# Kernel optimization log

Hardware: AMD Instinct MI355X
Metric: run time of the kernel (lower is better)

## Reference

```python
import jax, jax.numpy as jnp
import numpy as np

N_USERS, N_MOVIES, D, E, C = 100000, 50000, 128, 1000000, 5


def setup_inputs() -> dict:
    key = jax.random.key(0)
    ks = jax.random.split(key, 6)
    ufeat = jax.random.normal(ks[0], (N_USERS, D), dtype=jnp.float32)
    ifeat = jax.random.normal(ks[1], (N_MOVIES, D), dtype=jnp.float32)
    # Xavier-uniform init, PyTorch Linear layout [out, in]
    b1 = float(np.sqrt(6.0 / (2 * D + D)))
    W1 = jax.random.uniform(ks[2], (D, 2 * D), dtype=jnp.float32, minval=-b1, maxval=b1)
    b2 = float(np.sqrt(6.0 / (D + C)))
    W2 = jax.random.uniform(ks[3], (C, D), dtype=jnp.float32, minval=-b2, maxval=b2)
    src_idx = jax.random.randint(ks[4], (E,), 0, N_USERS, dtype=jnp.int64 if jax.config.jax_enable_x64 else jnp.int32)
    dst_idx = jax.random.randint(ks[5], (E,), 0, N_MOVIES, dtype=jnp.int64 if jax.config.jax_enable_x64 else jnp.int32)
    return {"ufeat": ufeat, "ifeat": ifeat, "W1": W1, "W2": W2,
            "src_idx": src_idx, "dst_idx": dst_idx}


def reference(ufeat, ifeat, W1, W2, src_idx, dst_idx):
    # Gather per-edge source (user) and destination (movie) features.
    h_u = ufeat[src_idx]            # [E, D]
    h_v = ifeat[dst_idx]            # [E, D]
    h = jnp.concatenate([h_u, h_v], axis=1)      # [E, 2D]
    # Linear(2D->D, no bias) -> ReLU -> Linear(D->C, no bias)
    hidden = jax.nn.relu(h @ W1.T)               # [E, D]
    score = hidden @ W2.T                        # [E, C]
    return score
```

## Files before the change

kernel.cpp:

```cpp
#include <hip/hip_runtime.h>
#include <hip/hip_fp16.h>

#define D 128
#define C 5

typedef _Float16 half8 __attribute__((ext_vector_type(8)));
typedef float f32x4 __attribute__((ext_vector_type(4)));
typedef float f32x8 __attribute__((ext_vector_type(8)));

__global__ __launch_bounds__(256) void convert_weights(
    const float* __restrict__ W1, const float* __restrict__ W2,
    _Float16* __restrict__ W1h, _Float16* __restrict__ W2h)
{
    int idx = blockIdx.x * 256 + threadIdx.x;
    if (idx < D * 2 * D) {
        W1h[idx] = (_Float16)W1[idx];
    } else {
        int j = idx - D * 2 * D;
        if (j < 16 * D) {
            int r = j >> 7;
            int k = j & 127;
            W2h[j] = (_Float16)((r < C) ? W2[r * D + k] : 0.f);
        }
    }
}

__global__ __launch_bounds__(256) void precompute_uv(
    const float* __restrict__ ufeat, const float* __restrict__ ifeat,
    const _Float16* __restrict__ W1h, _Float16* __restrict__ U,
    _Float16* __restrict__ V, int n_users, int n_movies, int groupsU)
{
    __shared__ _Float16 ldsB[128 * 128];
    char* lb = (char*)ldsB;

    int gid = blockIdx.x;
    const float* feat;
    _Float16* out;
    int off, base_row, nrows;
    if (gid < groupsU) {
        feat = ufeat; out = U; off = 0;
        base_row = gid * 128; nrows = n_users;
    } else {
        feat = ifeat; out = V; off = D;
        base_row = (gid - groupsU) * 128; nrows = n_movies;
    }

    int tid = threadIdx.x;
    int w = tid >> 6;
    int l = tid & 63;
    int row16 = l & 15;
    int kg = l >> 4;

    int rbase = base_row + w * 32;
    half8 afrag[2][4];
    #pragma unroll
    for (int t = 0; t < 2; ++t) {
        int ra = rbase + t * 16 + row16;
        int rc = (ra < nrows) ? ra : (nrows - 1);
        const float* fp = feat + (size_t)rc * D + kg * 8;
        #pragma unroll
        for (int kb = 0; kb < 4; ++kb) {
            f32x8 f = *reinterpret_cast<const f32x8*>(&fp[kb * 32]);
            afrag[t][kb] = __builtin_convertvector(f, half8);
        }
    }

    {
        const char* wbase = (const char*)W1h + off * 2;
        #pragma unroll
        for (int i = 0; i < 8; ++i) {
            int lin = (tid + i * 256) * 16;
            int col = lin >> 8;
            int within = lin & 255;
            const char* srcp = wbase + (size_t)col * 512 + within;
            int dstb = lin ^ ((col & 7) << 4);
            *reinterpret_cast<uint4*>(lb + dstb) =
                *reinterpret_cast<const uint4*>(srcp);
        }
    }
    __syncthreads();

    #pragma unroll 2
    for (int jt = 0; jt < 8; ++jt) {
        int col = jt * 16 + row16;
        int sw = (col & 7) << 4;
        int bb = col * 256 + kg * 16;
        half8 b0 = *reinterpret_cast<const half8*>(lb + ((bb +   0) ^ sw));
        half8 b1 = *reinterpret_cast<const half8*>(lb + ((bb +  64) ^ sw));
        half8 b2 = *reinterpret_cast<const half8*>(lb + ((bb + 128) ^ sw));
        half8 b3 = *reinterpret_cast<const half8*>(lb + ((bb + 192) ^ sw));

        f32x4 acc0 = {0.f, 0.f, 0.f, 0.f};
        f32x4 acc1 = {0.f, 0.f, 0.f, 0.f};
        acc0 = __builtin_amdgcn_mfma_f32_16x16x32_f16(afrag[0][0], b0, acc0, 0, 0, 0);
        acc1 = __builtin_amdgcn_mfma_f32_16x16x32_f16(afrag[1][0], b0, acc1, 0, 0, 0);
        acc0 = __builtin_amdgcn_mfma_f32_16x16x32_f16(afrag[0][1], b1, acc0, 0, 0, 0);
        acc1 = __builtin_amdgcn_mfma_f32_16x16x32_f16(afrag[1][1], b1, acc1, 0, 0, 0);
        acc0 = __builtin_amdgcn_mfma_f32_16x16x32_f16(afrag[0][2], b2, acc0, 0, 0, 0);
        acc1 = __builtin_amdgcn_mfma_f32_16x16x32_f16(afrag[1][2], b2, acc1, 0, 0, 0);
        acc0 = __builtin_amdgcn_mfma_f32_16x16x32_f16(afrag[0][3], b3, acc0, 0, 0, 0);
        acc1 = __builtin_amdgcn_mfma_f32_16x16x32_f16(afrag[1][3], b3, acc1, 0, 0, 0);

        int r0 = rbase + kg * 4;
        #pragma unroll
        for (int j = 0; j < 4; ++j) {
            int r = r0 + j;
            if (r +  0 < nrows) out[(size_t)(r +  0) * D + col] = (_Float16)acc0[j];
            if (r + 16 < nrows) out[(size_t)(r + 16) * D + col] = (_Float16)acc1[j];
        }
    }
}

__global__ __launch_bounds__(256) void edge_mlp(
    const _Float16* __restrict__ U, const _Float16* __restrict__ V,
    const _Float16* __restrict__ W2h,
    const int* __restrict__ src, const int* __restrict__ dst,
    float* __restrict__ out, int E)
{
    int tid = threadIdx.x;
    int w = tid >> 6;
    int l = tid & 63;
    int base = blockIdx.x * 256 + w * 64;
    int row16 = l & 15;
    int kg = l >> 4;

    half8 bfrag[4];
    #pragma unroll
    for (int kb = 0; kb < 4; ++kb)
        bfrag[kb] = *reinterpret_cast<const half8*>(&W2h[row16 * D + kb * 32 + kg * 8]);

    int i64 = base + l;
    int ic = (i64 < E) ? i64 : (E - 1);
    int sv = src[ic];
    int dv = dst[ic];

    const _Float16* up[4];
    const _Float16* vp[4];
    #pragma unroll
    for (int g = 0; g < 4; ++g) {
        int sg_ = __shfl(sv, g * 16 + row16);
        int dg_ = __shfl(dv, g * 16 + row16);
        up[g] = &U[(size_t)sg_ * D + kg * 8];
        vp[g] = &V[(size_t)dg_ * D + kg * 8];
    }

    f32x4 acc[4];
    #pragma unroll
    for (int g = 0; g < 4; ++g) acc[g] = (f32x4){0.f, 0.f, 0.f, 0.f};

    #pragma unroll
    for (int kb = 0; kb < 4; ++kb) {
        half8 au0 = *reinterpret_cast<const half8*>(&up[0][kb * 32]);
        half8 av0 = *reinterpret_cast<const half8*>(&vp[0][kb * 32]);
        half8 au1 = *reinterpret_cast<const half8*>(&up[1][kb * 32]);
        half8 av1 = *reinterpret_cast<const half8*>(&vp[1][kb * 32]);
        half8 au2 = *reinterpret_cast<const half8*>(&up[2][kb * 32]);
        half8 av2 = *reinterpret_cast<const half8*>(&vp[2][kb * 32]);
        half8 au3 = *reinterpret_cast<const half8*>(&up[3][kb * 32]);
        half8 av3 = *reinterpret_cast<const half8*>(&vp[3][kb * 32]);
        half8 h0 = __builtin_elementwise_max(au0 + av0, (half8)(_Float16)0.f);
        half8 h1 = __builtin_elementwise_max(au1 + av1, (half8)(_Float16)0.f);
        half8 h2 = __builtin_elementwise_max(au2 + av2, (half8)(_Float16)0.f);
        half8 h3 = __builtin_elementwise_max(au3 + av3, (half8)(_Float16)0.f);
        acc[0] = __builtin_amdgcn_mfma_f32_16x16x32_f16(h0, bfrag[kb], acc[0], 0, 0, 0);
        acc[1] = __builtin_amdgcn_mfma_f32_16x16x32_f16(h1, bfrag[kb], acc[1], 0, 0, 0);
        acc[2] = __builtin_amdgcn_mfma_f32_16x16x32_f16(h2, bfrag[kb], acc[2], 0, 0, 0);
        acc[3] = __builtin_amdgcn_mfma_f32_16x16x32_f16(h3, bfrag[kb], acc[3], 0, 0, 0);
    }

    int col = row16;
    if (col < C) {
        #pragma unroll
        for (int g = 0; g < 4; ++g) {
            #pragma unroll
            for (int j = 0; j < 4; ++j) {
                int er = base + g * 16 + kg * 4 + j;
                if (er < E) out[(size_t)er * C + col] = acc[g][j];
            }
        }
    }
}

extern "C" void kernel_launch(void* const* d_in, const int* in_sizes, int n_in,
                              void* d_out, int out_size, void* d_ws, size_t ws_size,
                              hipStream_t stream) {
    (void)n_in; (void)out_size; (void)ws_size;
    const float* ufeat = (const float*)d_in[0];
    const float* ifeat = (const float*)d_in[1];
    const float* W1    = (const float*)d_in[2];
    const float* W2    = (const float*)d_in[3];
    const int*   src   = (const int*)d_in[4];
    const int*   dst   = (const int*)d_in[5];

    int n_users  = in_sizes[0] / D;
    int n_movies = in_sizes[1] / D;
    int E        = in_sizes[4];

    float* out = (float*)d_out;
    _Float16* Ubuf = (_Float16*)d_ws;
    _Float16* Vbuf = Ubuf + (size_t)n_users * D;
    _Float16* W2h  = Vbuf + (size_t)n_movies * D;
    _Float16* W1h  = W2h + 16 * D;

    convert_weights<<<(D * 2 * D + 16 * D + 255) / 256, 256, 0, stream>>>(
        W1, W2, W1h, W2h);

    int groupsU = (n_users + 127) / 128;
    int groupsV = (n_movies + 127) / 128;
    precompute_uv<<<groupsU + groupsV, 256, 0, stream>>>(
        ufeat, ifeat, W1h, Ubuf, Vbuf, n_users, n_movies, groupsU);

    int eblocks = (E + 255) / 256;
    edge_mlp<<<eblocks, 256, 0, stream>>>(Ubuf, Vbuf, W2h, src, dst, out, E);
}
```

Measured before the change: 104.7 us.

## Fuse weight conversion into consumers and transpose MFMA for vectorized U/V stores

Removes the separate convert_weights launch: precompute_uv now converts W1 from fp32 to fp16 while staging it into LDS, and edge_mlp converts W2 rows directly into register fragments, zeroing rows past C. The precompute MFMA operands are swapped so each lane holds four consecutive output columns of one row, so U/V are written as 8-byte half4 stores instead of scattered 2-byte stores. This saves a kernel launch and makes the output writes better coalesced, at the cost of reading fp32 weights twice as wide in each block.

After: 108.4 us. +3.5%, slower.

```diff
diff --git a/kernel.cpp b/kernel.cpp
--- a/kernel.cpp
+++ b/kernel.cpp
@@ -5,29 +5,13 @@
 #define C 5
 
 typedef _Float16 half8 __attribute__((ext_vector_type(8)));
+typedef _Float16 half4 __attribute__((ext_vector_type(4)));
 typedef float f32x4 __attribute__((ext_vector_type(4)));
 typedef float f32x8 __attribute__((ext_vector_type(8)));
 
-__global__ __launch_bounds__(256) void convert_weights(
-    const float* __restrict__ W1, const float* __restrict__ W2,
-    _Float16* __restrict__ W1h, _Float16* __restrict__ W2h)
-{
-    int idx = blockIdx.x * 256 + threadIdx.x;
-    if (idx < D * 2 * D) {
-        W1h[idx] = (_Float16)W1[idx];
-    } else {
-        int j = idx - D * 2 * D;
-        if (j < 16 * D) {
-            int r = j >> 7;
-            int k = j & 127;
-            W2h[j] = (_Float16)((r < C) ? W2[r * D + k] : 0.f);
-        }
-    }
-}
-
 __global__ __launch_bounds__(256) void precompute_uv(
     const float* __restrict__ ufeat, const float* __restrict__ ifeat,
-    const _Float16* __restrict__ W1h, _Float16* __restrict__ U,
+    const float* __restrict__ W1, _Float16* __restrict__ U,
     _Float16* __restrict__ V, int n_users, int n_movies, int groupsU)
 {
     __shared__ _Float16 ldsB[128 * 128];
@@ -66,54 +50,52 @@
     }
 
     {
-        const char* wbase = (const char*)W1h + off * 2;
+        const char* wbase = (const char*)W1 + (size_t)off * 4;
         #pragma unroll
         for (int i = 0; i < 8; ++i) {
             int lin = (tid + i * 256) * 16;
             int col = lin >> 8;
             int within = lin & 255;
-            const char* srcp = wbase + (size_t)col * 512 + within;
+            const float* srcp = reinterpret_cast<const float*>(
+                wbase + (size_t)col * 1024 + (size_t)within * 2);
+            f32x8 wv = *reinterpret_cast<const f32x8*>(srcp);
+            half8 hv = __builtin_convertvector(wv, half8);
             int dstb = lin ^ ((col & 7) << 4);
-            *reinterpret_cast<uint4*>(lb + dstb) =
-                *reinterpret_cast<const uint4*>(srcp);
+            *reinterpret_cast<half8*>(lb + dstb) = hv;
         }
     }
     __syncthreads();
 
     #pragma unroll 2
-    for (int jt = 0; jt < 8; ++jt) {
-        int col = jt * 16 + row16;
-        int sw = (col & 7) << 4;
-        int bb = col * 256 + kg * 16;
-        half8 b0 = *reinterpret_cast<const half8*>(lb + ((bb +   0) ^ sw));
-        half8 b1 = *reinterpret_cast<const half8*>(lb + ((bb +  64) ^ sw));
-        half8 b2 = *reinterpret_cast<const half8*>(lb + ((bb + 128) ^ sw));
-        half8 b3 = *reinterpret_cast<const half8*>(lb + ((bb + 192) ^ sw));
+    for (int ct = 0; ct < 8; ++ct) {
+        int c = ct * 16 + row16;
+        int sw = (c & 7) << 4;
+        int bb = c * 256 + kg * 16;
+        half8 w0 = *reinterpret_cast<const half8*>(lb + ((bb +   0) ^ sw));
+        half8 w1 = *reinterpret_cast<const half8*>(lb + ((bb +  64) ^ sw));
+        half8 w2 = *reinterpret_cast<const half8*>(lb + ((bb + 128) ^ sw));
+        half8 w3 = *reinterpret_cast<const half8*>(lb + ((bb + 192) ^ sw));
 
-        f32x4 acc0 = {0.f, 0.f, 0.f, 0.f};
-        f32x4 acc1 = {0.f, 0.f, 0.f, 0.f};
-        acc0 = __builtin_amdgcn_mfma_f32_16x16x32_f16(afrag[0][0], b0, acc0, 0, 0, 0);
-        acc1 = __builtin_amdgcn_mfma_f32_16x16x32_f16(afrag[1][0], b0, acc1, 0, 0, 0);
-        acc0 = __builtin_amdgcn_mfma_f32_16x16x32_f16(afrag[0][1], b1, acc0, 0, 0, 0);
-        acc1 = __builtin_amdgcn_mfma_f32_16x16x32_f16(afrag[1][1], b1, acc1, 0, 0, 0);
-        acc0 = __builtin_amdgcn_mfma_f32_16x16x32_f16(afrag[0][2], b2, acc0, 0, 0, 0);
-        acc1 = __builtin_amdgcn_mfma_f32_16x16x32_f16(afrag[1][2], b2, acc1, 0, 0, 0);
-        acc0 = __builtin_amdgcn_mfma_f32_16x16x32_f16(afrag[0][3], b3, acc0, 0, 0, 0);
-        acc1 = __builtin_amdgcn_mfma_f32_16x16x32_f16(afrag[1][3], b3, acc1, 0, 0, 0);
+        #pragma unroll
+        for (int rt = 0; rt < 2; ++rt) {
+            f32x4 acc = {0.f, 0.f, 0.f, 0.f};
+            acc = __builtin_amdgcn_mfma_f32_16x16x32_f16(w0, afrag[rt][0], acc, 0, 0, 0);
+            acc = __builtin_amdgcn_mfma_f32_16x16x32_f16(w1, afrag[rt][1], acc, 0, 0, 0);
+            acc = __builtin_amdgcn_mfma_f32_16x16x32_f16(w2, afrag[rt][2], acc, 0, 0, 0);
+            acc = __builtin_amdgcn_mfma_f32_16x16x32_f16(w3, afrag[rt][3], acc, 0, 0, 0);
 
-        int r0 = rbase + kg * 4;
-        #pragma unroll
-        for (int j = 0; j < 4; ++j) {
-            int r = r0 + j;
-            if (r +  0 < nrows) out[(size_t)(r +  0) * D + col] = (_Float16)acc0[j];
-            if (r + 16 < nrows) out[(size_t)(r + 16) * D + col] = (_Float16)acc1[j];
+            int r = rbase + rt * 16 + row16;
+            if (r < nrows) {
+                half4 hv = __builtin_convertvector(acc, half4);
+                *reinterpret_cast<half4*>(&out[(size_t)r * D + ct * 16 + kg * 4]) = hv;
+            }
         }
     }
 }
 
 __global__ __launch_bounds__(256) void edge_mlp(
     const _Float16* __restrict__ U, const _Float16* __restrict__ V,
-    const _Float16* __restrict__ W2h,
+    const float* __restrict__ W2,
     const int* __restrict__ src, const int* __restrict__ dst,
     float* __restrict__ out, int E)
 {
@@ -125,9 +107,16 @@
     int kg = l >> 4;
 
     half8 bfrag[4];
-    #pragma unroll
-    for (int kb = 0; kb < 4; ++kb)
-        bfrag[kb] = *reinterpret_cast<const half8*>(&W2h[row16 * D + kb * 32 + kg * 8]);
+    {
+        int rw = (row16 < C) ? row16 : 0;
+        const float* wp = &W2[(size_t)rw * D + kg * 8];
+        #pragma unroll
+        for (int kb = 0; kb < 4; ++kb) {
+            f32x8 wv = *reinterpret_cast<const f32x8*>(&wp[kb * 32]);
+            half8 h = __builtin_convertvector(wv, half8);
+            bfrag[kb] = (row16 < C) ? h : (half8)(_Float16)0.f;
+        }
+    }
 
     int i64 = base + l;
     int ic = (i64 < E) ? i64 : (E - 1);
@@ -199,17 +188,12 @@
     float* out = (float*)d_out;
     _Float16* Ubuf = (_Float16*)d_ws;
     _Float16* Vbuf = Ubuf + (size_t)n_users * D;
-    _Float16* W2h  = Vbuf + (size_t)n_movies * D;
-    _Float16* W1h  = W2h + 16 * D;
-
-    convert_weights<<<(D * 2 * D + 16 * D + 255) / 256, 256, 0, stream>>>(
-        W1, W2, W1h, W2h);
 
     int groupsU = (n_users + 127) / 128;
     int groupsV = (n_movies + 127) / 128;
     precompute_uv<<<groupsU + groupsV, 256, 0, stream>>>(
-        ufeat, ifeat, W1h, Ubuf, Vbuf, n_users, n_movies, groupsU);
+        ufeat, ifeat, W1, Ubuf, Vbuf, n_users, n_movies, groupsU);
 
     int eblocks = (E + 255) / 256;
-    edge_mlp<<<eblocks, 256, 0, stream>>>(Ubuf, Vbuf, W2h, src, dst, out, E);
+    edge_mlp<<<eblocks, 256, 0, stream>>>(Ubuf, Vbuf, W2, src, dst, out, E);
 }
```
